# Kernel optimization log

Hardware: AMD Instinct MI355X
Metric: run time of the kernel (lower is better)

## Reference

```python
import jax, jax.numpy as jnp
import numpy as np

N_NODES = 100000
N_EDGES = 3200000
LEAKY_SLOPE = 0.01  # torch F.leaky_relu default


def _conv(x, W, b, src, dst):
    # DGL-style custom GCN conv: sum-aggregate neighbor features, then linear.
    msgs = x[src]                                            # [E, d_in]
    agg = jax.ops.segment_sum(msgs, dst, num_segments=N_NODES)  # [N, d_in]
    return agg @ W + b                                       # [N, d_out]


def setup_inputs() -> dict:
    key = jax.random.key(0)
    ks = jax.random.split(key, 8)
    features = jax.random.normal(ks[0], (N_NODES, 4), dtype=jnp.float32)
    src = jax.random.randint(ks[1], (N_EDGES,), 0, N_NODES, dtype=jnp.int32)
    dst = jax.random.randint(ks[2], (N_EDGES,), 0, N_NODES, dtype=jnp.int32)
    # Kaiming-ish init scale
    W1 = jax.random.normal(ks[3], (4, 64), dtype=jnp.float32) * (1.0 / np.sqrt(4))
    b1 = jnp.zeros((64,), dtype=jnp.float32)
    W2 = jax.random.normal(ks[4], (64, 64), dtype=jnp.float32) * (1.0 / np.sqrt(64))
    b2 = jnp.zeros((64,), dtype=jnp.float32)
    W5 = jax.random.normal(ks[5], (64, 3), dtype=jnp.float32) * (1.0 / np.sqrt(64))
    b5 = jnp.zeros((3,), dtype=jnp.float32)
    return {"features": features, "src": src, "dst": dst,
            "W1": W1, "b1": b1, "W2": W2, "b2": b2, "W5": W5, "b5": b5}


def reference(features, src, dst, W1, b1, W2, b2, W5, b5):
    lrelu = lambda v: jax.nn.leaky_relu(v, negative_slope=LEAKY_SLOPE)
    x = lrelu(_conv(features, W1, b1, src, dst))
    # layer2 weights are shared across 7 applications (as in the torch module)
    for _ in range(7):
        x = lrelu(_conv(x, W2, b2, src, dst))
    x = _conv(x, W5, b5, src, dst)
    return x
```

## Files before the change

kernel.cpp:

```cpp
#include <hip/hip_runtime.h>

#define N_NODES 100000
#define N_EDGES 3200000
#define SLOPE 0.01f

#define NBUCK 391
#define NBLK_B 256
#define EPB (N_EDGES / NBLK_B)
#define NGH (NBUCK * NBLK_B)

typedef __attribute__((ext_vector_type(8))) short short8;
typedef __attribute__((ext_vector_type(4))) float f32x4;

static inline size_t align_up(size_t x, size_t a){ return (x + a - 1) / a * a; }

__device__ inline unsigned short f2bf(float f){
  unsigned u = __float_as_uint(f);
  u += 0x7fffu + ((u >> 16) & 1u);
  return (unsigned short)(u >> 16);
}
__device__ inline float bf2f(unsigned short s){
  return __uint_as_float(((unsigned)s) << 16);
}
__device__ inline void add2(float& a0, float& a1, unsigned u){
  a0 += __uint_as_float(u << 16);
  a1 += __uint_as_float(u & 0xffff0000u);
}


__global__ void gbhist_k(const int* __restrict__ dst, int* __restrict__ ghist){
  __shared__ int h[NBUCK];
  int tid = threadIdx.x, blk = blockIdx.x;
  for (int i = tid; i < NBUCK; i += 256) h[i] = 0;
  __syncthreads();
  int e0 = blk * EPB;
  for (int e = e0 + tid; e < e0 + EPB; e += 256) atomicAdd(&h[dst[e] >> 8], 1);
  __syncthreads();
  for (int i = tid; i < NBUCK; i += 256) ghist[i * NBLK_B + blk] = h[i];
}

__global__ void scan1_k(const int* __restrict__ in, int* __restrict__ out,
                        int* __restrict__ bsums, int n){
  __shared__ int lds[256];
  int tid = threadIdx.x;
  int base = blockIdx.x * 1024 + tid * 4;
  int v0 = (base + 0 < n) ? in[base + 0] : 0;
  int v1 = (base + 1 < n) ? in[base + 1] : 0;
  int v2 = (base + 2 < n) ? in[base + 2] : 0;
  int v3 = (base + 3 < n) ? in[base + 3] : 0;
  int tsum = v0 + v1 + v2 + v3;
  lds[tid] = tsum;
  for (int off = 1; off < 256; off <<= 1){
    __syncthreads();
    int x = (tid >= off) ? lds[tid - off] : 0;
    __syncthreads();
    lds[tid] += x;
  }
  __syncthreads();
  int excl = lds[tid] - tsum;
  if (base + 0 < n) out[base + 0] = excl;
  if (base + 1 < n) out[base + 1] = excl + v0;
  if (base + 2 < n) out[base + 2] = excl + v0 + v1;
  if (base + 3 < n) out[base + 3] = excl + v0 + v1 + v2;
  if (tid == 255) bsums[blockIdx.x] = lds[255];
}

__global__ void scan2_k(int* bsums, int nb){
  if (threadIdx.x == 0 && blockIdx.x == 0){
    int acc = 0;
    for (int i = 0; i < nb; i++){ int t = bsums[i]; bsums[i] = acc; acc += t; }
  }
}

__global__ void scan3_k(int* __restrict__ out, const int* __restrict__ bsums,
                        int n, int set_end){
  int i = blockIdx.x * 256 + threadIdx.x;
  if (i < n) out[i] += bsums[i >> 10];
  else if (i == n && set_end) out[n] = N_EDGES;
}

__global__ void passB_k(const int* __restrict__ src, const int* __restrict__ dst,
                        const int* __restrict__ goff, int* __restrict__ pk){
  __shared__ int cur[NBUCK];
  int tid = threadIdx.x, blk = blockIdx.x;
  for (int b = tid; b < NBUCK; b += 256) cur[b] = goff[b * NBLK_B + blk];
  __syncthreads();
  int e0 = blk * EPB;
  for (int e = e0 + tid; e < e0 + EPB; e += 256){
    int d = dst[e];
    int pos = atomicAdd(&cur[d >> 8], 1);
    pk[pos] = (src[e] << 8) | (d & 255);
  }
}

__global__ void histnode_k(const int* __restrict__ pk, const int* __restrict__ goff,
                           int* __restrict__ counts){
  __shared__ int cnt[256];
  int b = blockIdx.x, tid = threadIdx.x;
  cnt[tid] = 0;
  __syncthreads();
  int s = goff[b * NBLK_B];
  int e = (b == NBUCK - 1) ? N_EDGES : goff[(b + 1) * NBLK_B];
  for (int i = s + tid; i < e; i += 256) atomicAdd(&cnt[pk[i] & 255], 1);
  __syncthreads();
  int node = b * 256 + tid;
  if (node < N_NODES) counts[node] = cnt[tid];
}

__global__ void passC_k(const int* __restrict__ pk, const int* __restrict__ goff,
                        const int* __restrict__ row_ptr, int* __restrict__ ssrc){
  __shared__ int cur[256];
  int b = blockIdx.x, tid = threadIdx.x;
  int node = b * 256 + tid;
  if (node < N_NODES) cur[tid] = row_ptr[node];
  __syncthreads();
  int s = goff[b * NBLK_B];
  int e = (b == NBUCK - 1) ? N_EDGES : goff[(b + 1) * NBLK_B];
  for (int i = s + tid; i < e; i += 256){
    int v = pk[i];
    int p = atomicAdd(&cur[v & 255], 1);
    ssrc[p] = v >> 8;
  }
}

__global__ void conv1_k(const float* __restrict__ feat, const int* __restrict__ row_ptr,
                        const int* __restrict__ ssrc, const float* __restrict__ W1,
                        const float* __restrict__ b1, unsigned short* __restrict__ out){
  int gt = blockIdx.x * 256 + threadIdx.x;
  int node = gt >> 6;
  int lane = threadIdx.x & 63;
  int s = row_ptr[node], t = row_ptr[node + 1];
  float a0 = 0.f, a1 = 0.f, a2 = 0.f, a3 = 0.f;
  for (int i = s + lane; i < t; i += 64){
    int nb = ssrc[i];
    const float4 v = *(const float4*)(feat + (size_t)nb * 4);
    a0 += v.x; a1 += v.y; a2 += v.z; a3 += v.w;
  }
  for (int m = 1; m < 64; m <<= 1){
    a0 += __shfl_xor(a0, m);
    a1 += __shfl_xor(a1, m);
    a2 += __shfl_xor(a2, m);
    a3 += __shfl_xor(a3, m);
  }
  float o = b1[lane] + a0 * W1[lane] + a1 * W1[64 + lane] + a2 * W1[128 + lane] + a3 * W1[192 + lane];
  o = (o > 0.f) ? o : SLOPE * o;
  out[node * 64 + lane] = f2bf(o);
}

__global__ void mm64_k(const unsigned short* __restrict__ x, const float* __restrict__ W,
                       unsigned short* __restrict__ z){
  int lane = threadIdx.x & 63;
  int wid = (blockIdx.x * blockDim.x + threadIdx.x) >> 6;
  int nwaves = (gridDim.x * blockDim.x) >> 6;
  int r = lane & 15, g = lane >> 4;
  short8 Bf[4][2];
  #pragma unroll
  for (int nc = 0; nc < 4; ++nc)
    #pragma unroll
    for (int kt = 0; kt < 2; ++kt){
      short8 f;
      #pragma unroll
      for (int j = 0; j < 8; ++j){
        int k = kt * 32 + g * 8 + j;
        f[j] = (short)f2bf(W[k * 64 + nc * 16 + r]);
      }
      Bf[nc][kt] = f;
    }
  const int NT = N_NODES / 16;
  for (int t = wid; t < NT; t += nwaves){
    int base = t * 16;
    const short8 A0 = *(const short8*)(x + (size_t)(base + r) * 64 + g * 8);
    const short8 A1 = *(const short8*)(x + (size_t)(base + r) * 64 + 32 + g * 8);
    #pragma unroll
    for (int nc = 0; nc < 4; ++nc){
      f32x4 c = {0.f, 0.f, 0.f, 0.f};
      c = __builtin_amdgcn_mfma_f32_16x16x32_bf16(A0, Bf[nc][0], c, 0, 0, 0);
      c = __builtin_amdgcn_mfma_f32_16x16x32_bf16(A1, Bf[nc][1], c, 0, 0, 0);
      #pragma unroll
      for (int i = 0; i < 4; ++i){
        int row = g * 4 + i;
        z[(size_t)(base + row) * 64 + nc * 16 + r] = f2bf(c[i]);
      }
    }
  }
}

__global__ void agg64_k(const unsigned short* __restrict__ z, const int* __restrict__ row_ptr,
                        const int* __restrict__ ssrc, const float* __restrict__ b,
                        unsigned short* __restrict__ out){
  int gt = blockIdx.x * 256 + threadIdx.x;
  int node = gt >> 6;
  int lane = threadIdx.x & 63;
  int s = row_ptr[node], cnt = row_ptr[node + 1] - s;
  int nb_l = ssrc[s + lane];
  int q = lane >> 3, o = lane & 7;
  float a0=0.f,a1=0.f,a2=0.f,a3=0.f,a4=0.f,a5=0.f,a6=0.f,a7=0.f;
  uint4 v0, v1, v2, v3, v4, v5;
  int cm1 = (cnt > 0) ? cnt - 1 : 0;
  {
    int j0 = min( 0 + q, cm1), j1 = min( 8 + q, cm1), j2 = min(16 + q, cm1);
    int j3 = min(24 + q, cm1), j4 = min(32 + q, cm1), j5 = min(40 + q, cm1);
    int n0 = __shfl(nb_l, j0), n1 = __shfl(nb_l, j1), n2 = __shfl(nb_l, j2);
    int n3 = __shfl(nb_l, j3), n4 = __shfl(nb_l, j4), n5 = __shfl(nb_l, j5);
    const size_t oo = (size_t)(o << 3);
    v0 = *(const uint4*)(z + (size_t)n0 * 64 + oo);
    v1 = *(const uint4*)(z + (size_t)n1 * 64 + oo);
    v2 = *(const uint4*)(z + (size_t)n2 * 64 + oo);
    v3 = *(const uint4*)(z + (size_t)n3 * 64 + oo);
    v4 = *(const uint4*)(z + (size_t)n4 * 64 + oo);
    v5 = *(const uint4*)(z + (size_t)n5 * 64 + oo);
  }
  if ( 0 + q < cnt){ add2(a0,a1,v0.x); add2(a2,a3,v0.y); add2(a4,a5,v0.z); add2(a6,a7,v0.w); }
  if ( 8 + q < cnt){ add2(a0,a1,v1.x); add2(a2,a3,v1.y); add2(a4,a5,v1.z); add2(a6,a7,v1.w); }
  if (16 + q < cnt){ add2(a0,a1,v2.x); add2(a2,a3,v2.y); add2(a4,a5,v2.z); add2(a6,a7,v2.w); }
  if (24 + q < cnt){ add2(a0,a1,v3.x); add2(a2,a3,v3.y); add2(a4,a5,v3.z); add2(a6,a7,v3.w); }
  if (32 + q < cnt){ add2(a0,a1,v4.x); add2(a2,a3,v4.y); add2(a4,a5,v4.z); add2(a6,a7,v4.w); }
  if (40 + q < cnt){ add2(a0,a1,v5.x); add2(a2,a3,v5.y); add2(a4,a5,v5.z); add2(a6,a7,v5.w); }
  for (int i = 48 + q; i < cnt; i += 8){
    int nb = ssrc[s + i];
    uint4 vv = *(const uint4*)(z + (size_t)nb * 64 + (size_t)(o << 3));
    add2(a0,a1,vv.x); add2(a2,a3,vv.y); add2(a4,a5,vv.z); add2(a6,a7,vv.w);
  }
  for (int m = 8; m < 64; m <<= 1){
    a0 += __shfl_xor(a0, m); a1 += __shfl_xor(a1, m);
    a2 += __shfl_xor(a2, m); a3 += __shfl_xor(a3, m);
    a4 += __shfl_xor(a4, m); a5 += __shfl_xor(a5, m);
    a6 += __shfl_xor(a6, m); a7 += __shfl_xor(a7, m);
  }
  if (lane < 8){
    const float4 bA = *(const float4*)(b + lane * 8);
    const float4 bB = *(const float4*)(b + lane * 8 + 4);
    float y0 = a0 + bA.x, y1 = a1 + bA.y, y2 = a2 + bA.z, y3 = a3 + bA.w;
    float y4 = a4 + bB.x, y5 = a5 + bB.y, y6 = a6 + bB.z, y7 = a7 + bB.w;
    y0 = (y0 > 0.f) ? y0 : SLOPE * y0;  y1 = (y1 > 0.f) ? y1 : SLOPE * y1;
    y2 = (y2 > 0.f) ? y2 : SLOPE * y2;  y3 = (y3 > 0.f) ? y3 : SLOPE * y3;
    y4 = (y4 > 0.f) ? y4 : SLOPE * y4;  y5 = (y5 > 0.f) ? y5 : SLOPE * y5;
    y6 = (y6 > 0.f) ? y6 : SLOPE * y6;  y7 = (y7 > 0.f) ? y7 : SLOPE * y7;
    uint4 pkd;
    pkd.x = (unsigned)f2bf(y0) | ((unsigned)f2bf(y1) << 16);
    pkd.y = (unsigned)f2bf(y2) | ((unsigned)f2bf(y3) << 16);
    pkd.z = (unsigned)f2bf(y4) | ((unsigned)f2bf(y5) << 16);
    pkd.w = (unsigned)f2bf(y6) | ((unsigned)f2bf(y7) << 16);
    *(uint4*)(out + (size_t)node * 64 + lane * 8) = pkd;
  }
}

__global__ void premult_k(const unsigned short* __restrict__ x, const float* __restrict__ W5,
                          float* __restrict__ y){
  int gt = blockIdx.x * 256 + threadIdx.x;
  int node = gt >> 6;
  int lane = threadIdx.x & 63;
  float xv = bf2f(x[node * 64 + lane]);
  float p0 = xv * W5[lane * 3 + 0];
  float p1 = xv * W5[lane * 3 + 1];
  float p2 = xv * W5[lane * 3 + 2];
  for (int m = 1; m < 64; m <<= 1){
    p0 += __shfl_xor(p0, m);
    p1 += __shfl_xor(p1, m);
    p2 += __shfl_xor(p2, m);
  }
  if (lane == 0){
    y[node * 3 + 0] = p0;
    y[node * 3 + 1] = p1;
    y[node * 3 + 2] = p2;
  }
}

__global__ void agg3_k(const float* __restrict__ y, const int* __restrict__ row_ptr,
                       const int* __restrict__ ssrc, const float* __restrict__ b5,
                       float* __restrict__ out){
  int gt = blockIdx.x * 256 + threadIdx.x;
  int node = gt >> 6;
  int lane = threadIdx.x & 63;
  int s = row_ptr[node], t = row_ptr[node + 1];
  int c = lane & 3;
  float acc = 0.f;
  if (c < 3){
    for (int i = s + (lane >> 2); i < t; i += 16) acc += y[(size_t)ssrc[i] * 3 + c];
  }
  for (int m = 4; m < 64; m <<= 1) acc += __shfl_xor(acc, m);
  if (lane < 3) out[node * 3 + lane] = acc + b5[lane];
}


extern "C" void kernel_launch(void* const* d_in, const int* in_sizes, int n_in,
                              void* d_out, int out_size, void* d_ws, size_t ws_size,
                              hipStream_t stream){
  const float* feat = (const float*)d_in[0];
  const int*   src  = (const int*)d_in[1];
  const int*   dst  = (const int*)d_in[2];
  const float* W1   = (const float*)d_in[3];
  const float* b1   = (const float*)d_in[4];
  const float* W2   = (const float*)d_in[5];
  const float* b2   = (const float*)d_in[6];
  const float* W5   = (const float*)d_in[7];
  const float* b5   = (const float*)d_in[8];
  float* out = (float*)d_out;

  char* p = (char*)d_ws;
  auto carve = [&](size_t bytes) -> char* {
    char* r = p; p += align_up(bytes, 512); return r;
  };
  int*   counts  = (int*)carve((size_t)N_NODES * 4);
  int*   row_ptr = (int*)carve((size_t)(N_NODES + 1) * 4);
  int*   bsums   = (int*)carve(128 * 4);
  int*   ghist   = (int*)carve((size_t)NGH * 4);
  int*   goff    = (int*)carve((size_t)NGH * 4);
  int*   ssrc    = (int*)carve(((size_t)N_EDGES + 64) * 4);
  unsigned short* bufA = (unsigned short*)carve((size_t)N_NODES * 64 * 2);
  unsigned short* bufB = (unsigned short*)carve((size_t)N_NODES * 64 * 2);
  float* y3      = (float*)carve((size_t)N_NODES * 3 * 4);
  int*   pk      = (int*)carve((size_t)N_EDGES * 4);
  unsigned short* zbuf = (unsigned short*)pk;

  gbhist_k<<<NBLK_B, 256, 0, stream>>>(dst, ghist);
  {
    int nb = (NGH + 1023) / 1024;
    scan1_k<<<nb, 256, 0, stream>>>(ghist, goff, bsums, NGH);
    scan2_k<<<1, 64, 0, stream>>>(bsums, nb);
    scan3_k<<<(NGH + 256) / 256, 256, 0, stream>>>(goff, bsums, NGH, 0);
  }
  passB_k<<<NBLK_B, 256, 0, stream>>>(src, dst, goff, pk);
  histnode_k<<<NBUCK, 256, 0, stream>>>(pk, goff, counts);
  {
    int nb = (N_NODES + 1023) / 1024;
    scan1_k<<<nb, 256, 0, stream>>>(counts, row_ptr, bsums, N_NODES);
    scan2_k<<<1, 64, 0, stream>>>(bsums, nb);
    scan3_k<<<(N_NODES + 256) / 256, 256, 0, stream>>>(row_ptr, bsums, N_NODES, 1);
  }
  passC_k<<<NBUCK, 256, 0, stream>>>(pk, goff, row_ptr, ssrc);
  hipMemsetAsync(ssrc + N_EDGES, 0, 64 * 4, stream);

  conv1_k<<<(N_NODES * 64) / 256, 256, 0, stream>>>(feat, row_ptr, ssrc, W1, b1, bufA);

  unsigned short* xin = bufA;
  unsigned short* xout = bufB;
  for (int l = 0; l < 7; ++l){
    mm64_k<<<256, 256, 0, stream>>>(xin, W2, zbuf);
    agg64_k<<<(N_NODES * 64) / 256, 256, 0, stream>>>(zbuf, row_ptr, ssrc, b2, xout);
    unsigned short* tmp = xin; xin = xout; xout = tmp;
  }

  premult_k<<<(N_NODES * 64) / 256, 256, 0, stream>>>(xin, W5, y3);
  agg3_k<<<(N_NODES * 64) / 256, 256, 0, stream>>>(y3, row_ptr, ssrc, b5, out);
}
```

Measured before the change: 620.7 us.

## Rework aggregation to two nodes per wave, transpose MFMA, widen scans and bucket passes

Several changes are bundled. The hot agg64 kernel now handles two nodes per wavefront, with each lane owning two feature columns and running an unrolled loop over neighbours, replacing the 8-way split with shuffle reductions. mm64 swaps the MFMA operands so each lane stores four contiguous bf16 outputs. The scan's block-sum step becomes a wave-parallel scan, and the histogram passes use more blocks and threads. The final 3-wide output is padded to 4 floats for aligned gathers. Risks include lower memory-level parallelism per node in the gather and divergence between two nodes with different degrees.

```diff
diff --git a/kernel.cpp b/kernel.cpp
--- a/kernel.cpp
+++ b/kernel.cpp
@@ -5,12 +5,13 @@
 #define SLOPE 0.01f
 
 #define NBUCK 391
-#define NBLK_B 256
+#define NBLK_B 1024
 #define EPB (N_EDGES / NBLK_B)
 #define NGH (NBUCK * NBLK_B)
 
 typedef __attribute__((ext_vector_type(8))) short short8;
 typedef __attribute__((ext_vector_type(4))) float f32x4;
+typedef __attribute__((ext_vector_type(2))) float f32x2;
 
 static inline size_t align_up(size_t x, size_t a){ return (x + a - 1) / a * a; }
 
@@ -21,10 +22,6 @@
 }
 __device__ inline float bf2f(unsigned short s){
   return __uint_as_float(((unsigned)s) << 16);
-}
-__device__ inline void add2(float& a0, float& a1, unsigned u){
-  a0 += __uint_as_float(u << 16);
-  a1 += __uint_as_float(u & 0xffff0000u);
 }
 
 
@@ -66,9 +63,19 @@
 }
 
 __global__ void scan2_k(int* bsums, int nb){
-  if (threadIdx.x == 0 && blockIdx.x == 0){
-    int acc = 0;
-    for (int i = 0; i < nb; i++){ int t = bsums[i]; bsums[i] = acc; acc += t; }
+  int lane = threadIdx.x;
+  int base = 0;
+  for (int off = 0; off < nb; off += 64){
+    int idx = off + lane;
+    int v = (idx < nb) ? bsums[idx] : 0;
+    int sc = v;
+    for (int m = 1; m < 64; m <<= 1){
+      int t = __shfl_up(sc, m);
+      if (lane >= m) sc += t;
+    }
+    int total = __shfl(sc, 63);
+    if (idx < nb) bsums[idx] = sc - v + base;
+    base += total;
   }
 }
 
@@ -97,14 +104,14 @@
                            int* __restrict__ counts){
   __shared__ int cnt[256];
   int b = blockIdx.x, tid = threadIdx.x;
-  cnt[tid] = 0;
+  if (tid < 256) cnt[tid] = 0;
   __syncthreads();
   int s = goff[b * NBLK_B];
   int e = (b == NBUCK - 1) ? N_EDGES : goff[(b + 1) * NBLK_B];
-  for (int i = s + tid; i < e; i += 256) atomicAdd(&cnt[pk[i] & 255], 1);
+  for (int i = s + tid; i < e; i += 512) atomicAdd(&cnt[pk[i] & 255], 1);
   __syncthreads();
   int node = b * 256 + tid;
-  if (node < N_NODES) counts[node] = cnt[tid];
+  if (tid < 256 && node < N_NODES) counts[node] = cnt[tid];
 }
 
 __global__ void passC_k(const int* __restrict__ pk, const int* __restrict__ goff,
@@ -112,11 +119,11 @@
   __shared__ int cur[256];
   int b = blockIdx.x, tid = threadIdx.x;
   int node = b * 256 + tid;
-  if (node < N_NODES) cur[tid] = row_ptr[node];
+  if (tid < 256 && node < N_NODES) cur[tid] = row_ptr[node];
   __syncthreads();
   int s = goff[b * NBLK_B];
   int e = (b == NBUCK - 1) ? N_EDGES : goff[(b + 1) * NBLK_B];
-  for (int i = s + tid; i < e; i += 256){
+  for (int i = s + tid; i < e; i += 512){
     int v = pk[i];
     int p = atomicAdd(&cur[v & 255], 1);
     ssrc[p] = v >> 8;
@@ -153,34 +160,32 @@
   int wid = (blockIdx.x * blockDim.x + threadIdx.x) >> 6;
   int nwaves = (gridDim.x * blockDim.x) >> 6;
   int r = lane & 15, g = lane >> 4;
-  short8 Bf[4][2];
+  short8 Af[4][2];
   #pragma unroll
-  for (int nc = 0; nc < 4; ++nc)
+  for (int mb = 0; mb < 4; ++mb)
     #pragma unroll
     for (int kt = 0; kt < 2; ++kt){
       short8 f;
       #pragma unroll
       for (int j = 0; j < 8; ++j){
         int k = kt * 32 + g * 8 + j;
-        f[j] = (short)f2bf(W[k * 64 + nc * 16 + r]);
+        f[j] = (short)f2bf(W[k * 64 + mb * 16 + r]);
       }
-      Bf[nc][kt] = f;
+      Af[mb][kt] = f;
     }
   const int NT = N_NODES / 16;
   for (int t = wid; t < NT; t += nwaves){
     int base = t * 16;
-    const short8 A0 = *(const short8*)(x + (size_t)(base + r) * 64 + g * 8);
-    const short8 A1 = *(const short8*)(x + (size_t)(base + r) * 64 + 32 + g * 8);
+    const short8 B0 = *(const short8*)(x + (size_t)(base + r) * 64 + g * 8);
+    const short8 B1 = *(const short8*)(x + (size_t)(base + r) * 64 + 32 + g * 8);
     #pragma unroll
-    for (int nc = 0; nc < 4; ++nc){
+    for (int mb = 0; mb < 4; ++mb){
       f32x4 c = {0.f, 0.f, 0.f, 0.f};
-      c = __builtin_amdgcn_mfma_f32_16x16x32_bf16(A0, Bf[nc][0], c, 0, 0, 0);
-      c = __builtin_amdgcn_mfma_f32_16x16x32_bf16(A1, Bf[nc][1], c, 0, 0, 0);
-      #pragma unroll
-      for (int i = 0; i < 4; ++i){
-        int row = g * 4 + i;
-        z[(size_t)(base + row) * 64 + nc * 16 + r] = f2bf(c[i]);
-      }
+      c = __builtin_amdgcn_mfma_f32_16x16x32_bf16(Af[mb][0], B0, c, 0, 0, 0);
+      c = __builtin_amdgcn_mfma_f32_16x16x32_bf16(Af[mb][1], B1, c, 0, 0, 0);
+      ushort4 pk4;
+      pk4.x = f2bf(c[0]); pk4.y = f2bf(c[1]); pk4.z = f2bf(c[2]); pk4.w = f2bf(c[3]);
+      *(ushort4*)(z + (size_t)(base + r) * 64 + mb * 16 + g * 4) = pk4;
     }
   }
 }
@@ -189,64 +194,54 @@
                         const int* __restrict__ ssrc, const float* __restrict__ b,
                         unsigned short* __restrict__ out){
   int gt = blockIdx.x * 256 + threadIdx.x;
-  int node = gt >> 6;
-  int lane = threadIdx.x & 63;
-  int s = row_ptr[node], cnt = row_ptr[node + 1] - s;
-  int nb_l = ssrc[s + lane];
-  int q = lane >> 3, o = lane & 7;
-  float a0=0.f,a1=0.f,a2=0.f,a3=0.f,a4=0.f,a5=0.f,a6=0.f,a7=0.f;
-  uint4 v0, v1, v2, v3, v4, v5;
-  int cm1 = (cnt > 0) ? cnt - 1 : 0;
-  {
-    int j0 = min( 0 + q, cm1), j1 = min( 8 + q, cm1), j2 = min(16 + q, cm1);
-    int j3 = min(24 + q, cm1), j4 = min(32 + q, cm1), j5 = min(40 + q, cm1);
-    int n0 = __shfl(nb_l, j0), n1 = __shfl(nb_l, j1), n2 = __shfl(nb_l, j2);
-    int n3 = __shfl(nb_l, j3), n4 = __shfl(nb_l, j4), n5 = __shfl(nb_l, j5);
-    const size_t oo = (size_t)(o << 3);
-    v0 = *(const uint4*)(z + (size_t)n0 * 64 + oo);
-    v1 = *(const uint4*)(z + (size_t)n1 * 64 + oo);
-    v2 = *(const uint4*)(z + (size_t)n2 * 64 + oo);
-    v3 = *(const uint4*)(z + (size_t)n3 * 64 + oo);
-    v4 = *(const uint4*)(z + (size_t)n4 * 64 + oo);
-    v5 = *(const uint4*)(z + (size_t)n5 * 64 + oo);
-  }
-  if ( 0 + q < cnt){ add2(a0,a1,v0.x); add2(a2,a3,v0.y); add2(a4,a5,v0.z); add2(a6,a7,v0.w); }
-  if ( 8 + q < cnt){ add2(a0,a1,v1.x); add2(a2,a3,v1.y); add2(a4,a5,v1.z); add2(a6,a7,v1.w); }
-  if (16 + q < cnt){ add2(a0,a1,v2.x); add2(a2,a3,v2.y); add2(a4,a5,v2.z); add2(a6,a7,v2.w); }
-  if (24 + q < cnt){ add2(a0,a1,v3.x); add2(a2,a3,v3.y); add2(a4,a5,v3.z); add2(a6,a7,v3.w); }
-  if (32 + q < cnt){ add2(a0,a1,v4.x); add2(a2,a3,v4.y); add2(a4,a5,v4.z); add2(a6,a7,v4.w); }
-  if (40 + q < cnt){ add2(a0,a1,v5.x); add2(a2,a3,v5.y); add2(a4,a5,v5.z); add2(a6,a7,v5.w); }
-  for (int i = 48 + q; i < cnt; i += 8){
-    int nb = ssrc[s + i];
-    uint4 vv = *(const uint4*)(z + (size_t)nb * 64 + (size_t)(o << 3));
-    add2(a0,a1,vv.x); add2(a2,a3,vv.y); add2(a4,a5,vv.z); add2(a6,a7,vv.w);
-  }
-  for (int m = 8; m < 64; m <<= 1){
-    a0 += __shfl_xor(a0, m); a1 += __shfl_xor(a1, m);
-    a2 += __shfl_xor(a2, m); a3 += __shfl_xor(a3, m);
-    a4 += __shfl_xor(a4, m); a5 += __shfl_xor(a5, m);
-    a6 += __shfl_xor(a6, m); a7 += __shfl_xor(a7, m);
-  }
-  if (lane < 8){
-    const float4 bA = *(const float4*)(b + lane * 8);
-    const float4 bB = *(const float4*)(b + lane * 8 + 4);
-    float y0 = a0 + bA.x, y1 = a1 + bA.y, y2 = a2 + bA.z, y3 = a3 + bA.w;
-    float y4 = a4 + bB.x, y5 = a5 + bB.y, y6 = a6 + bB.z, y7 = a7 + bB.w;
-    y0 = (y0 > 0.f) ? y0 : SLOPE * y0;  y1 = (y1 > 0.f) ? y1 : SLOPE * y1;
-    y2 = (y2 > 0.f) ? y2 : SLOPE * y2;  y3 = (y3 > 0.f) ? y3 : SLOPE * y3;
-    y4 = (y4 > 0.f) ? y4 : SLOPE * y4;  y5 = (y5 > 0.f) ? y5 : SLOPE * y5;
-    y6 = (y6 > 0.f) ? y6 : SLOPE * y6;  y7 = (y7 > 0.f) ? y7 : SLOPE * y7;
-    uint4 pkd;
-    pkd.x = (unsigned)f2bf(y0) | ((unsigned)f2bf(y1) << 16);
-    pkd.y = (unsigned)f2bf(y2) | ((unsigned)f2bf(y3) << 16);
-    pkd.z = (unsigned)f2bf(y4) | ((unsigned)f2bf(y5) << 16);
-    pkd.w = (unsigned)f2bf(y6) | ((unsigned)f2bf(y7) << 16);
-    *(uint4*)(out + (size_t)node * 64 + lane * 8) = pkd;
-  }
+  int wv = gt >> 6;
+  int lane = threadIdx.x & 63;
+  int cl = lane & 31;
+  int node = wv * 2 + (lane >> 5);
+  int s = row_ptr[node];
+  int cnt = row_ptr[node + 1] - s;
+  int ocnt = __shfl_xor(cnt, 32);
+  int minc = __builtin_amdgcn_readfirstlane(min(cnt, ocnt));
+  int maxc = __builtin_amdgcn_readfirstlane(max(cnt, ocnt));
+  int cm1 = (cnt > 0) ? (cnt - 1) : 0;
+  const size_t co = (size_t)(cl << 1);
+  f32x2 a; a.x = 0.f; a.y = 0.f;
+  int i = 0;
+  for (; i + 4 <= minc; i += 4){
+    int i0 = ssrc[s + i], i1 = ssrc[s + i + 1], i2 = ssrc[s + i + 2], i3 = ssrc[s + i + 3];
+    unsigned u0 = *(const unsigned*)(z + (size_t)i0 * 64 + co);
+    unsigned u1 = *(const unsigned*)(z + (size_t)i1 * 64 + co);
+    unsigned u2 = *(const unsigned*)(z + (size_t)i2 * 64 + co);
+    unsigned u3 = *(const unsigned*)(z + (size_t)i3 * 64 + co);
+    f32x2 t0, t1, t2, t3;
+    t0.x = __uint_as_float(u0 << 16); t0.y = __uint_as_float(u0 & 0xffff0000u);
+    t1.x = __uint_as_float(u1 << 16); t1.y = __uint_as_float(u1 & 0xffff0000u);
+    t2.x = __uint_as_float(u2 << 16); t2.y = __uint_as_float(u2 & 0xffff0000u);
+    t3.x = __uint_as_float(u3 << 16); t3.y = __uint_as_float(u3 & 0xffff0000u);
+    a += t0; a += t1; a += t2; a += t3;
+  }
+  for (; i < maxc; i += 4){
+    #pragma unroll
+    for (int k2 = 0; k2 < 4; ++k2){
+      int ii = i + k2;
+      int j = min(ii, cm1);
+      int idx = ssrc[s + j];
+      unsigned u = *(const unsigned*)(z + (size_t)idx * 64 + co);
+      u = (ii < cnt) ? u : 0u;
+      f32x2 t; t.x = __uint_as_float(u << 16); t.y = __uint_as_float(u & 0xffff0000u);
+      a += t;
+    }
+  }
+  const f32x2 bb = *(const f32x2*)(b + (cl << 1));
+  float yx = a.x + bb.x, yy = a.y + bb.y;
+  yx = (yx > 0.f) ? yx : SLOPE * yx;
+  yy = (yy > 0.f) ? yy : SLOPE * yy;
+  unsigned pkd = (unsigned)f2bf(yx) | ((unsigned)f2bf(yy) << 16);
+  *(unsigned*)(out + (size_t)node * 64 + (cl << 1)) = pkd;
 }
 
 __global__ void premult_k(const unsigned short* __restrict__ x, const float* __restrict__ W5,
-                          float* __restrict__ y){
+                          float* __restrict__ y4){
   int gt = blockIdx.x * 256 + threadIdx.x;
   int node = gt >> 6;
   int lane = threadIdx.x & 63;
@@ -260,13 +255,12 @@
     p2 += __shfl_xor(p2, m);
   }
   if (lane == 0){
-    y[node * 3 + 0] = p0;
-    y[node * 3 + 1] = p1;
-    y[node * 3 + 2] = p2;
-  }
-}
-
-__global__ void agg3_k(const float* __restrict__ y, const int* __restrict__ row_ptr,
+    float4 v; v.x = p0; v.y = p1; v.z = p2; v.w = 0.f;
+    *(float4*)(y4 + (size_t)node * 4) = v;
+  }
+}
+
+__global__ void agg3_k(const float* __restrict__ y4, const int* __restrict__ row_ptr,
                        const int* __restrict__ ssrc, const float* __restrict__ b5,
                        float* __restrict__ out){
   int gt = blockIdx.x * 256 + threadIdx.x;
@@ -275,9 +269,7 @@
   int s = row_ptr[node], t = row_ptr[node + 1];
   int c = lane & 3;
   float acc = 0.f;
-  if (c < 3){
-    for (int i = s + (lane >> 2); i < t; i += 16) acc += y[(size_t)ssrc[i] * 3 + c];
-  }
+  for (int i = s + (lane >> 2); i < t; i += 16) acc += y4[(size_t)ssrc[i] * 4 + c];
   for (int m = 4; m < 64; m <<= 1) acc += __shfl_xor(acc, m);
   if (lane < 3) out[node * 3 + lane] = acc + b5[lane];
 }
@@ -303,32 +295,32 @@
   };
   int*   counts  = (int*)carve((size_t)N_NODES * 4);
   int*   row_ptr = (int*)carve((size_t)(N_NODES + 1) * 4);
-  int*   bsums   = (int*)carve(128 * 4);
+  int*   bsums   = (int*)carve(512 * 4);
   int*   ghist   = (int*)carve((size_t)NGH * 4);
   int*   goff    = (int*)carve((size_t)NGH * 4);
   int*   ssrc    = (int*)carve(((size_t)N_EDGES + 64) * 4);
   unsigned short* bufA = (unsigned short*)carve((size_t)N_NODES * 64 * 2);
   unsigned short* bufB = (unsigned short*)carve((size_t)N_NODES * 64 * 2);
-  float* y3      = (float*)carve((size_t)N_NODES * 3 * 4);
+  float* y4      = (float*)carve((size_t)N_NODES * 4 * 4);
   int*   pk      = (int*)carve((size_t)N_EDGES * 4);
   unsigned short* zbuf = (unsigned short*)pk;
 
   gbhist_k<<<NBLK_B, 256, 0, stream>>>(dst, ghist);
   {
-    int nb = (NGH + 1023) / 1024;
+    int nb = NGH / 1024;
     scan1_k<<<nb, 256, 0, stream>>>(ghist, goff, bsums, NGH);
     scan2_k<<<1, 64, 0, stream>>>(bsums, nb);
     scan3_k<<<(NGH + 256) / 256, 256, 0, stream>>>(goff, bsums, NGH, 0);
   }
   passB_k<<<NBLK_B, 256, 0, stream>>>(src, dst, goff, pk);
-  histnode_k<<<NBUCK, 256, 0, stream>>>(pk, goff, counts);
+  histnode_k<<<NBUCK, 512, 0, stream>>>(pk, goff, counts);
   {
     int nb = (N_NODES + 1023) / 1024;
     scan1_k<<<nb, 256, 0, stream>>>(counts, row_ptr, bsums, N_NODES);
     scan2_k<<<1, 64, 0, stream>>>(bsums, nb);
     scan3_k<<<(N_NODES + 256) / 256, 256, 0, stream>>>(row_ptr, bsums, N_NODES, 1);
   }
-  passC_k<<<NBUCK, 256, 0, stream>>>(pk, goff, row_ptr, ssrc);
+  passC_k<<<NBUCK, 512, 0, stream>>>(pk, goff, row_ptr, ssrc);
   hipMemsetAsync(ssrc + N_EDGES, 0, 64 * 4, stream);
 
   conv1_k<<<(N_NODES * 64) / 256, 256, 0, stream>>>(feat, row_ptr, ssrc, W1, b1, bufA);
@@ -336,11 +328,11 @@
   unsigned short* xin = bufA;
   unsigned short* xout = bufB;
   for (int l = 0; l < 7; ++l){
-    mm64_k<<<256, 256, 0, stream>>>(xin, W2, zbuf);
-    agg64_k<<<(N_NODES * 64) / 256, 256, 0, stream>>>(zbuf, row_ptr, ssrc, b2, xout);
+    mm64_k<<<512, 256, 0, stream>>>(xin, W2, zbuf);
+    agg64_k<<<N_NODES / 8, 256, 0, stream>>>(zbuf, row_ptr, ssrc, b2, xout);
     unsigned short* tmp = xin; xin = xout; xout = tmp;
   }
 
-  premult_k<<<(N_NODES * 64) / 256, 256, 0, stream>>>(xin, W5, y3);
-  agg3_k<<<(N_NODES * 64) / 256, 256, 0, stream>>>(y3, row_ptr, ssrc, b5, out);
-}
+  premult_k<<<(N_NODES * 64) / 256, 256, 0, stream>>>(xin, W5, y4);
+  agg3_k<<<(N_NODES * 64) / 256, 256, 0, stream>>>(y4, row_ptr, ssrc, b5, out);
+}
```

Result: slower. 669.3 us (+7.8%).

## Stage CSR build scatters in LDS, transpose MFMA output, pad final features

Applied to the files above, without the earlier changes.

The bucket scatter in passB is now staged in shared memory (local histogram, wave scan, then coalesced per-bucket copy-out), and passC sorts each bucket locally into an LDS buffer with a fallback to direct global writes on overflow, dropping the row_ptr dependency. The scan2 serial loop becomes a wave-level shuffle scan. mm64 swaps the MFMA operands so each lane writes four contiguous bf16 outputs instead of scattered 2-byte stores. The final 3-wide features are padded to float4 for aligned gathers, and several launch sizes are doubled. The LDS buffers raise shared-memory use and may lower occupancy.

```diff
diff --git a/kernel.cpp b/kernel.cpp
--- a/kernel.cpp
+++ b/kernel.cpp
@@ -8,6 +8,7 @@
 #define NBLK_B 256
 #define EPB (N_EDGES / NBLK_B)
 #define NGH (NBUCK * NBLK_B)
+#define CAP_C 10240
 
 typedef __attribute__((ext_vector_type(8))) short short8;
 typedef __attribute__((ext_vector_type(4))) float f32x4;
@@ -66,9 +67,19 @@
 }
 
 __global__ void scan2_k(int* bsums, int nb){
-  if (threadIdx.x == 0 && blockIdx.x == 0){
-    int acc = 0;
-    for (int i = 0; i < nb; i++){ int t = bsums[i]; bsums[i] = acc; acc += t; }
+  int lane = threadIdx.x;
+  int base = 0;
+  for (int off = 0; off < nb; off += 64){
+    int idx = off + lane;
+    int v = (idx < nb) ? bsums[idx] : 0;
+    int sc = v;
+    for (int m = 1; m < 64; m <<= 1){
+      int t = __shfl_up(sc, m);
+      if (lane >= m) sc += t;
+    }
+    int total = __shfl(sc, 63);
+    if (idx < nb) bsums[idx] = sc - v + base;
+    base += total;
   }
 }
 
@@ -81,15 +92,42 @@
 
 __global__ void passB_k(const int* __restrict__ src, const int* __restrict__ dst,
                         const int* __restrict__ goff, int* __restrict__ pk){
-  __shared__ int cur[NBUCK];
+  __shared__ int h[NBUCK];
+  __shared__ int buf[EPB];
   int tid = threadIdx.x, blk = blockIdx.x;
-  for (int b = tid; b < NBUCK; b += 256) cur[b] = goff[b * NBLK_B + blk];
+  for (int i = tid; i < NBUCK; i += 256) h[i] = 0;
   __syncthreads();
   int e0 = blk * EPB;
+  for (int e = e0 + tid; e < e0 + EPB; e += 256) atomicAdd(&h[dst[e] >> 8], 1);
+  __syncthreads();
+  if (tid < 64){
+    int base = 0;
+    for (int off = 0; off < NBUCK; off += 64){
+      int idx = off + tid;
+      int v = (idx < NBUCK) ? h[idx] : 0;
+      int sc = v;
+      for (int m = 1; m < 64; m <<= 1){
+        int t = __shfl_up(sc, m);
+        if (tid >= m) sc += t;
+      }
+      int total = __shfl(sc, 63);
+      if (idx < NBUCK) h[idx] = sc - v + base;
+      base += total;
+    }
+  }
+  __syncthreads();
   for (int e = e0 + tid; e < e0 + EPB; e += 256){
     int d = dst[e];
-    int pos = atomicAdd(&cur[d >> 8], 1);
-    pk[pos] = (src[e] << 8) | (d & 255);
+    int p = atomicAdd(&h[d >> 8], 1);
+    buf[p] = (src[e] << 8) | (d & 255);
+  }
+  __syncthreads();
+  int wv = tid >> 6, ln = tid & 63;
+  for (int b = wv; b < NBUCK; b += 4){
+    int s0 = (b == 0) ? 0 : h[b - 1];
+    int L  = h[b] - s0;
+    int g0 = goff[b * NBLK_B + blk];
+    for (int j = ln; j < L; j += 64) pk[g0 + j] = buf[s0 + j];
   }
 }
 
@@ -97,30 +135,53 @@
                            int* __restrict__ counts){
   __shared__ int cnt[256];
   int b = blockIdx.x, tid = threadIdx.x;
-  cnt[tid] = 0;
+  if (tid < 256) cnt[tid] = 0;
   __syncthreads();
   int s = goff[b * NBLK_B];
   int e = (b == NBUCK - 1) ? N_EDGES : goff[(b + 1) * NBLK_B];
-  for (int i = s + tid; i < e; i += 256) atomicAdd(&cnt[pk[i] & 255], 1);
+  for (int i = s + tid; i < e; i += 512) atomicAdd(&cnt[pk[i] & 255], 1);
   __syncthreads();
   int node = b * 256 + tid;
-  if (node < N_NODES) counts[node] = cnt[tid];
+  if (tid < 256 && node < N_NODES) counts[node] = cnt[tid];
 }
 
 __global__ void passC_k(const int* __restrict__ pk, const int* __restrict__ goff,
-                        const int* __restrict__ row_ptr, int* __restrict__ ssrc){
+                        int* __restrict__ ssrc){
   __shared__ int cur[256];
+  __shared__ int buf[CAP_C];
   int b = blockIdx.x, tid = threadIdx.x;
-  int node = b * 256 + tid;
-  if (node < N_NODES) cur[tid] = row_ptr[node];
+  if (tid < 256) cur[tid] = 0;
   __syncthreads();
   int s = goff[b * NBLK_B];
   int e = (b == NBUCK - 1) ? N_EDGES : goff[(b + 1) * NBLK_B];
-  for (int i = s + tid; i < e; i += 256){
+  int cnt = e - s;
+  for (int i = s + tid; i < e; i += 512) atomicAdd(&cur[pk[i] & 255], 1);
+  __syncthreads();
+  if (tid < 64){
+    int base = 0;
+    for (int off = 0; off < 256; off += 64){
+      int idx = off + tid;
+      int v = cur[idx];
+      int sc = v;
+      for (int m = 1; m < 64; m <<= 1){
+        int t = __shfl_up(sc, m);
+        if (tid >= m) sc += t;
+      }
+      int total = __shfl(sc, 63);
+      cur[idx] = sc - v + base;
+      base += total;
+    }
+  }
+  __syncthreads();
+  for (int i = s + tid; i < e; i += 512){
     int v = pk[i];
     int p = atomicAdd(&cur[v & 255], 1);
-    ssrc[p] = v >> 8;
-  }
+    if (p < CAP_C) buf[p] = v >> 8;
+    else ssrc[s + p] = v >> 8;
+  }
+  __syncthreads();
+  int lim = (cnt < CAP_C) ? cnt : CAP_C;
+  for (int i = tid; i < lim; i += 512) ssrc[s + i] = buf[i];
 }
 
 __global__ void conv1_k(const float* __restrict__ feat, const int* __restrict__ row_ptr,
@@ -153,34 +214,32 @@
   int wid = (blockIdx.x * blockDim.x + threadIdx.x) >> 6;
   int nwaves = (gridDim.x * blockDim.x) >> 6;
   int r = lane & 15, g = lane >> 4;
-  short8 Bf[4][2];
+  short8 Af[4][2];
   #pragma unroll
-  for (int nc = 0; nc < 4; ++nc)
+  for (int mb = 0; mb < 4; ++mb)
     #pragma unroll
     for (int kt = 0; kt < 2; ++kt){
       short8 f;
       #pragma unroll
       for (int j = 0; j < 8; ++j){
         int k = kt * 32 + g * 8 + j;
-        f[j] = (short)f2bf(W[k * 64 + nc * 16 + r]);
+        f[j] = (short)f2bf(W[k * 64 + mb * 16 + r]);
       }
-      Bf[nc][kt] = f;
+      Af[mb][kt] = f;
     }
   const int NT = N_NODES / 16;
   for (int t = wid; t < NT; t += nwaves){
     int base = t * 16;
-    const short8 A0 = *(const short8*)(x + (size_t)(base + r) * 64 + g * 8);
-    const short8 A1 = *(const short8*)(x + (size_t)(base + r) * 64 + 32 + g * 8);
+    const short8 B0 = *(const short8*)(x + (size_t)(base + r) * 64 + g * 8);
+    const short8 B1 = *(const short8*)(x + (size_t)(base + r) * 64 + 32 + g * 8);
     #pragma unroll
-    for (int nc = 0; nc < 4; ++nc){
+    for (int mb = 0; mb < 4; ++mb){
       f32x4 c = {0.f, 0.f, 0.f, 0.f};
-      c = __builtin_amdgcn_mfma_f32_16x16x32_bf16(A0, Bf[nc][0], c, 0, 0, 0);
-      c = __builtin_amdgcn_mfma_f32_16x16x32_bf16(A1, Bf[nc][1], c, 0, 0, 0);
-      #pragma unroll
-      for (int i = 0; i < 4; ++i){
-        int row = g * 4 + i;
-        z[(size_t)(base + row) * 64 + nc * 16 + r] = f2bf(c[i]);
-      }
+      c = __builtin_amdgcn_mfma_f32_16x16x32_bf16(Af[mb][0], B0, c, 0, 0, 0);
+      c = __builtin_amdgcn_mfma_f32_16x16x32_bf16(Af[mb][1], B1, c, 0, 0, 0);
+      ushort4 pk4;
+      pk4.x = f2bf(c[0]); pk4.y = f2bf(c[1]); pk4.z = f2bf(c[2]); pk4.w = f2bf(c[3]);
+      *(ushort4*)(z + (size_t)(base + r) * 64 + mb * 16 + g * 4) = pk4;
     }
   }
 }
@@ -246,7 +305,7 @@
 }
 
 __global__ void premult_k(const unsigned short* __restrict__ x, const float* __restrict__ W5,
-                          float* __restrict__ y){
+                          float* __restrict__ y4){
   int gt = blockIdx.x * 256 + threadIdx.x;
   int node = gt >> 6;
   int lane = threadIdx.x & 63;
@@ -260,13 +319,12 @@
     p2 += __shfl_xor(p2, m);
   }
   if (lane == 0){
-    y[node * 3 + 0] = p0;
-    y[node * 3 + 1] = p1;
-    y[node * 3 + 2] = p2;
-  }
-}
-
-__global__ void agg3_k(const float* __restrict__ y, const int* __restrict__ row_ptr,
+    float4 v; v.x = p0; v.y = p1; v.z = p2; v.w = 0.f;
+    *(float4*)(y4 + (size_t)node * 4) = v;
+  }
+}
+
+__global__ void agg3_k(const float* __restrict__ y4, const int* __restrict__ row_ptr,
                        const int* __restrict__ ssrc, const float* __restrict__ b5,
                        float* __restrict__ out){
   int gt = blockIdx.x * 256 + threadIdx.x;
@@ -275,9 +333,7 @@
   int s = row_ptr[node], t = row_ptr[node + 1];
   int c = lane & 3;
   float acc = 0.f;
-  if (c < 3){
-    for (int i = s + (lane >> 2); i < t; i += 16) acc += y[(size_t)ssrc[i] * 3 + c];
-  }
+  for (int i = s + (lane >> 2); i < t; i += 16) acc += y4[(size_t)ssrc[i] * 4 + c];
   for (int m = 4; m < 64; m <<= 1) acc += __shfl_xor(acc, m);
   if (lane < 3) out[node * 3 + lane] = acc + b5[lane];
 }
@@ -303,13 +359,13 @@
   };
   int*   counts  = (int*)carve((size_t)N_NODES * 4);
   int*   row_ptr = (int*)carve((size_t)(N_NODES + 1) * 4);
-  int*   bsums   = (int*)carve(128 * 4);
+  int*   bsums   = (int*)carve(512 * 4);
   int*   ghist   = (int*)carve((size_t)NGH * 4);
   int*   goff    = (int*)carve((size_t)NGH * 4);
   int*   ssrc    = (int*)carve(((size_t)N_EDGES + 64) * 4);
   unsigned short* bufA = (unsigned short*)carve((size_t)N_NODES * 64 * 2);
   unsigned short* bufB = (unsigned short*)carve((size_t)N_NODES * 64 * 2);
-  float* y3      = (float*)carve((size_t)N_NODES * 3 * 4);
+  float* y4      = (float*)carve((size_t)N_NODES * 4 * 4);
   int*   pk      = (int*)carve((size_t)N_EDGES * 4);
   unsigned short* zbuf = (unsigned short*)pk;
 
@@ -321,14 +377,14 @@
     scan3_k<<<(NGH + 256) / 256, 256, 0, stream>>>(goff, bsums, NGH, 0);
   }
   passB_k<<<NBLK_B, 256, 0, stream>>>(src, dst, goff, pk);
-  histnode_k<<<NBUCK, 256, 0, stream>>>(pk, goff, counts);
+  histnode_k<<<NBUCK, 512, 0, stream>>>(pk, goff, counts);
   {
     int nb = (N_NODES + 1023) / 1024;
     scan1_k<<<nb, 256, 0, stream>>>(counts, row_ptr, bsums, N_NODES);
     scan2_k<<<1, 64, 0, stream>>>(bsums, nb);
     scan3_k<<<(N_NODES + 256) / 256, 256, 0, stream>>>(row_ptr, bsums, N_NODES, 1);
   }
-  passC_k<<<NBUCK, 256, 0, stream>>>(pk, goff, row_ptr, ssrc);
+  passC_k<<<NBUCK, 512, 0, stream>>>(pk, goff, ssrc);
   hipMemsetAsync(ssrc + N_EDGES, 0, 64 * 4, stream);
 
   conv1_k<<<(N_NODES * 64) / 256, 256, 0, stream>>>(feat, row_ptr, ssrc, W1, b1, bufA);
@@ -336,11 +392,11 @@
   unsigned short* xin = bufA;
   unsigned short* xout = bufB;
   for (int l = 0; l < 7; ++l){
-    mm64_k<<<256, 256, 0, stream>>>(xin, W2, zbuf);
+    mm64_k<<<512, 256, 0, stream>>>(xin, W2, zbuf);
     agg64_k<<<(N_NODES * 64) / 256, 256, 0, stream>>>(zbuf, row_ptr, ssrc, b2, xout);
     unsigned short* tmp = xin; xin = xout; xout = tmp;
   }
 
-  premult_k<<<(N_NODES * 64) / 256, 256, 0, stream>>>(xin, W5, y3);
-  agg3_k<<<(N_NODES * 64) / 256, 256, 0, stream>>>(y3, row_ptr, ssrc, b5, out);
-}
+  premult_k<<<(N_NODES * 64) / 256, 256, 0, stream>>>(xin, W5, y4);
+  agg3_k<<<(N_NODES * 64) / 256, 256, 0, stream>>>(y4, row_ptr, ssrc, b5, out);
+}
```

New measurement: 633.2 us. +2.0%, slower.
